# Kernel tuning notes

Measured on AMD Instinct MI355X. Metric: run time of the kernel, lower is better.

Reference implementation:

```python
import jax, jax.numpy as jnp
import numpy as np

N_BINS = 100
LOWER, UPPER = 0.0, 1.0


def setup_inputs() -> dict:
    key = jax.random.key(0)
    outputs = jax.random.uniform(key, (96, 512, 512), dtype=jnp.float32)
    # bin boundaries, identical to np.linspace(lower - 1e-6, upper, n_bins + 1)
    bounds = jnp.asarray(np.linspace(LOWER - 1e-6, UPPER, N_BINS + 1), dtype=jnp.float32)
    return {"outputs": outputs, "bounds": bounds}


def reference(outputs, bounds):
    """Histogram counts: count[i] = #{x : bounds[i] < x <= bounds[i+1]}.

    Single-pass bucketize + scatter-add, replacing the original per-bin
    mask-and-sum loop with identical math (open-left, closed-right bins).
    """
    n_bins = bounds.shape[0] - 1
    x = outputs.ravel()
    # side='left': smallest i with bounds[i] >= x, i.e. bounds[i-1] < x <= bounds[i]
    bins = jnp.searchsorted(bounds, x, side="left") - 1
    valid = (bins >= 0) & (bins < n_bins)
    bins_c = jnp.where(valid, bins, n_bins)  # route out-of-range to dummy bin
    ones = jnp.where(valid, 1.0, 0.0).astype(outputs.dtype)
    count = jnp.zeros(n_bins + 1, dtype=outputs.dtype).at[bins_c].add(ones)
    return count[:n_bins]
```

## Files before the change

kernel.cpp:

```cpp
#include <hip/hip_runtime.h>

#define N_BINS 100
#define BLOCK 1024
#define GRID 512
#define EPS 1e-4f

__global__ __launch_bounds__(BLOCK) void hist_kernel(const float* __restrict__ x,
                                                     const float* __restrict__ bounds,
                                                     float* __restrict__ out,
                                                     int n) {
    __shared__ float sb[N_BINS + 1];
    __shared__ unsigned int sh[N_BINS][32];

    const int tid = threadIdx.x;
    const int col = tid & 31;

    if (tid < N_BINS + 1) sb[tid] = bounds[tid];
    for (int i = tid; i < N_BINS * 32; i += BLOCK) ((unsigned int*)sh)[i] = 0u;
    __syncthreads();

    const float b0 = sb[0];
    const float bN = sb[N_BINS];
    const float scale = (float)N_BINS / (bN - b0);
    const float c0 = -b0 * scale;

    const int n4 = n >> 2;
    const float4* __restrict__ x4 = (const float4*)x;
    const int gstride = GRID * BLOCK;
    int i = blockIdx.x * BLOCK + tid;

    if (i < n4) {
        float4 v = x4[i];
        for (;;) {
            const int inext = i + gstride;
            const bool more = inext < n4;
            float4 vn = v;
            if (more) vn = x4[inext];

            float f0 = fmaf(v.x, scale, c0);
            float f1 = fmaf(v.y, scale, c0);
            float f2 = fmaf(v.z, scale, c0);
            float f3 = fmaf(v.w, scale, c0);
            bool unc = (fabsf(f0 - rintf(f0)) < EPS) | (fabsf(f1 - rintf(f1)) < EPS) |
                       (fabsf(f2 - rintf(f2)) < EPS) | (fabsf(f3 - rintf(f3)) < EPS);

            if (__any(unc)) {
                float vals[4] = {v.x, v.y, v.z, v.w};
                #pragma unroll
                for (int k = 0; k < 4; ++k) {
                    float val = vals[k];
                    int g = min(max((int)fmaf(val, scale, c0), 0), N_BINS - 1);
                    while (g > 0 && val <= sb[g]) --g;
                    while (g < N_BINS - 1 && val > sb[g + 1]) ++g;
                    if (val > b0 && val <= bN) atomicAdd(&sh[g][col], 1u);
                }
            } else {
                float fs[4] = {f0, f1, f2, f3};
                #pragma unroll
                for (int k = 0; k < 4; ++k) {
                    float f = fs[k];
                    int g = min(max((int)f, 0), N_BINS - 1);
                    unsigned int inc = (f > 0.0f && f < (float)N_BINS) ? 1u : 0u;
                    atomicAdd(&sh[g][col], inc);
                }
            }

            if (!more) break;
            v = vn;
            i = inext;
        }
    }

    for (int t = (n4 << 2) + blockIdx.x * BLOCK + tid; t < n; t += gstride) {
        float val = x[t];
        int g = min(max((int)fmaf(val, scale, c0), 0), N_BINS - 1);
        while (g > 0 && val <= sb[g]) --g;
        while (g < N_BINS - 1 && val > sb[g + 1]) ++g;
        if (val > b0 && val <= bN) atomicAdd(&sh[g][col], 1u);
    }

    __syncthreads();
    if (tid < N_BINS) {
        unsigned int c = 0;
        #pragma unroll
        for (int j = 0; j < 32; ++j) c += sh[tid][(j + tid) & 31];
        atomicAdd(&out[tid], (float)c);
    }
}

extern "C" void kernel_launch(void* const* d_in, const int* in_sizes, int n_in,
                              void* d_out, int out_size, void* d_ws, size_t ws_size,
                              hipStream_t stream) {
    const float* x = (const float*)d_in[0];
    const float* bounds = (const float*)d_in[1];
    float* out = (float*)d_out;
    const int n = in_sizes[0];

    hipMemsetAsync(d_out, 0, out_size * sizeof(float), stream);
    hist_kernel<<<GRID, BLOCK, 0, stream>>>(x, bounds, out, n);
}
```

Baseline: 149.0 us.

## Batch four float4 loads per iteration, shrink blocks, simplify fast-path binning

The block size drops from 1024 to 256 threads, the grid grows from 512 to 2048 blocks, and launch bounds now request 8 blocks per CU. The grid-stride loop loads four float4 values up front and then processes them, replacing the one-ahead prefetch, so more loads are in flight to hide memory latency. The fast path drops the clamp and zero-increment atomics by sending values near the edges of the range to the slow exact path. This adds register pressure and shared-memory histogram setup per block (four times as many blocks), and relies on the widened uncertainty check to keep indices in range.

```diff
diff --git a/kernel.cpp b/kernel.cpp
--- a/kernel.cpp
+++ b/kernel.cpp
@@ -1,14 +1,14 @@
 #include <hip/hip_runtime.h>
 
 #define N_BINS 100
-#define BLOCK 1024
-#define GRID 512
+#define BLOCK 256
+#define GRID 2048
 #define EPS 1e-4f
 
-__global__ __launch_bounds__(BLOCK) void hist_kernel(const float* __restrict__ x,
-                                                     const float* __restrict__ bounds,
-                                                     float* __restrict__ out,
-                                                     int n) {
+__global__ __launch_bounds__(BLOCK, 8) void hist_kernel(const float* __restrict__ x,
+                                                        const float* __restrict__ bounds,
+                                                        float* __restrict__ out,
+                                                        int n) {
     __shared__ float sb[N_BINS + 1];
     __shared__ unsigned int sh[N_BINS][32];
 
@@ -19,57 +19,53 @@
     for (int i = tid; i < N_BINS * 32; i += BLOCK) ((unsigned int*)sh)[i] = 0u;
     __syncthreads();
 
-    const float b0 = sb[0];
-    const float bN = sb[N_BINS];
+    const float b0 = sb[0], bN = sb[N_BINS];
     const float scale = (float)N_BINS / (bN - b0);
     const float c0 = -b0 * scale;
+
+    auto proc4 = [&](float4 v) {
+        float f0 = fmaf(v.x, scale, c0);
+        float f1 = fmaf(v.y, scale, c0);
+        float f2 = fmaf(v.z, scale, c0);
+        float f3 = fmaf(v.w, scale, c0);
+        bool unc = (fabsf(f0 - rintf(f0)) < EPS) | (f0 <= EPS) | (f0 >= (float)N_BINS - EPS) |
+                   (fabsf(f1 - rintf(f1)) < EPS) | (f1 <= EPS) | (f1 >= (float)N_BINS - EPS) |
+                   (fabsf(f2 - rintf(f2)) < EPS) | (f2 <= EPS) | (f2 >= (float)N_BINS - EPS) |
+                   (fabsf(f3 - rintf(f3)) < EPS) | (f3 <= EPS) | (f3 >= (float)N_BINS - EPS);
+        if (__any(unc)) {
+            float vals[4] = {v.x, v.y, v.z, v.w};
+            #pragma unroll
+            for (int k = 0; k < 4; ++k) {
+                float val = vals[k];
+                int g = min(max((int)fmaf(val, scale, c0), 0), N_BINS - 1);
+                while (g > 0 && val <= sb[g]) --g;
+                while (g < N_BINS - 1 && val > sb[g + 1]) ++g;
+                if (val > b0 && val <= bN) atomicAdd(&sh[g][col], 1u);
+            }
+        } else {
+            atomicAdd(&sh[(int)f0][col], 1u);
+            atomicAdd(&sh[(int)f1][col], 1u);
+            atomicAdd(&sh[(int)f2][col], 1u);
+            atomicAdd(&sh[(int)f3][col], 1u);
+        }
+    };
 
     const int n4 = n >> 2;
     const float4* __restrict__ x4 = (const float4*)x;
     const int gstride = GRID * BLOCK;
     int i = blockIdx.x * BLOCK + tid;
 
-    if (i < n4) {
-        float4 v = x4[i];
-        for (;;) {
-            const int inext = i + gstride;
-            const bool more = inext < n4;
-            float4 vn = v;
-            if (more) vn = x4[inext];
-
-            float f0 = fmaf(v.x, scale, c0);
-            float f1 = fmaf(v.y, scale, c0);
-            float f2 = fmaf(v.z, scale, c0);
-            float f3 = fmaf(v.w, scale, c0);
-            bool unc = (fabsf(f0 - rintf(f0)) < EPS) | (fabsf(f1 - rintf(f1)) < EPS) |
-                       (fabsf(f2 - rintf(f2)) < EPS) | (fabsf(f3 - rintf(f3)) < EPS);
-
-            if (__any(unc)) {
-                float vals[4] = {v.x, v.y, v.z, v.w};
-                #pragma unroll
-                for (int k = 0; k < 4; ++k) {
-                    float val = vals[k];
-                    int g = min(max((int)fmaf(val, scale, c0), 0), N_BINS - 1);
-                    while (g > 0 && val <= sb[g]) --g;
-                    while (g < N_BINS - 1 && val > sb[g + 1]) ++g;
-                    if (val > b0 && val <= bN) atomicAdd(&sh[g][col], 1u);
-                }
-            } else {
-                float fs[4] = {f0, f1, f2, f3};
-                #pragma unroll
-                for (int k = 0; k < 4; ++k) {
-                    float f = fs[k];
-                    int g = min(max((int)f, 0), N_BINS - 1);
-                    unsigned int inc = (f > 0.0f && f < (float)N_BINS) ? 1u : 0u;
-                    atomicAdd(&sh[g][col], inc);
-                }
-            }
-
-            if (!more) break;
-            v = vn;
-            i = inext;
-        }
+    for (; i + 3 * gstride < n4; i += 4 * gstride) {
+        float4 v0 = x4[i];
+        float4 v1 = x4[i + gstride];
+        float4 v2 = x4[i + 2 * gstride];
+        float4 v3 = x4[i + 3 * gstride];
+        proc4(v0);
+        proc4(v1);
+        proc4(v2);
+        proc4(v3);
     }
+    for (; i < n4; i += gstride) proc4(x4[i]);
 
     for (int t = (n4 << 2) + blockIdx.x * BLOCK + tid; t < n; t += gstride) {
         float val = x[t];
```

Result: slower. 178.2 us (+19.5%).
